# Optimization experiments

Hardware: AMD Instinct MI355X
Metric: run time of the kernel (lower is better)

The kernel has to match this reference:

```python
import jax, jax.numpy as jnp
import numpy as np

EPS_BN = 1e-5
HEADS = 4
K = 16

def _bn_eval(x, g, b, m, v):
    # eval-mode BatchNorm1d over the feature (last) axis
    return (x - m) * (g / jnp.sqrt(v + EPS_BN)) + b

def setup_inputs() -> dict:
    key = jax.random.key(0)
    ks = jax.random.split(key, 32)
    B, T, N, C = 8, 4, 2048, 11
    D = 64
    hd = D // HEADS
    s = 0.05
    rn = lambda k, shp: jax.random.normal(k, shp, jnp.float32) * s
    inp = {
        'x': jax.random.normal(ks[0], (B, T, N, C), jnp.float32),
        # PointEmbedding: Linear(11,32) + BN(32) + ReLU + Linear(32,64) + BN(64) + ReLU
        'emb_w1': rn(ks[1], (32, C)), 'emb_b1': rn(ks[2], (32,)),
        'bn1_g': jnp.ones((32,)), 'bn1_b': jnp.zeros((32,)),
        'bn1_m': rn(ks[3], (32,)), 'bn1_v': jnp.ones((32,)),
        'emb_w2': rn(ks[4], (D, 32)), 'emb_b2': rn(ks[5], (D,)),
        'bn2_g': jnp.ones((D,)), 'bn2_b': jnp.zeros((D,)),
        'bn2_m': rn(ks[6], (D,)), 'bn2_v': jnp.ones((D,)),
        # DenseGATLayer
        'gat_W': rn(ks[7], (D, D)),          # Linear(64,64,bias=False)
        'att': rn(ks[8], (HEADS, 2 * hd)),    # attention vector per head
        # TemporalCrossAttention
        'q_w': rn(ks[9], (D, D)), 'q_b': rn(ks[10], (D,)),
        'kv_w': rn(ks[11], (D, D)), 'kv_b': rn(ks[12], (D,)),
        # heads
        'lw1': rn(ks[13], (32, D)), 'lb1': rn(ks[14], (32,)),
        'lw2': rn(ks[15], (4, 32)), 'lb2': rn(ks[16], (4,)),
        'rw1': rn(ks[17], (32, D)), 'rb1': rn(ks[18], (32,)),
        'rw2': rn(ks[19], (4, 32)), 'rb2': rn(ks[20], (4,)),
    }
    return inp

def _forward(x, emb_w1, emb_b1, bn1_g, bn1_b, bn1_m, bn1_v,
             emb_w2, emb_b2, bn2_g, bn2_b, bn2_m, bn2_v,
             gat_W, att, q_w, q_b, kv_w, kv_b,
             lw1, lb1, lw2, lb2, rw1, rb1, rw2, rb2):
    B, T, N, C = x.shape
    D = gat_W.shape[0]
    hd = D // HEADS
    BT = B * T
    xf = x.reshape(BT, N, C)

    # ---- PointEmbedding (BN in eval mode) ----
    h = xf @ emb_w1.T + emb_b1
    h = jax.nn.relu(_bn_eval(h, bn1_g, bn1_b, bn1_m, bn1_v))
    h = h @ emb_w2.T + emb_b2
    h = jax.nn.relu(_bn_eval(h, bn2_g, bn2_b, bn2_m, bn2_v))  # [BT,N,D]

    # ---- DenseGATLayer ----
    pos = xf[:, :, :2]  # raw xy
    sq = jnp.sum(pos * pos, axis=-1)  # [BT,N]
    d2 = sq[:, :, None] + sq[:, None, :] - 2.0 * jnp.einsum('bnc,bmc->bnm', pos, pos)
    _, idx = jax.lax.top_k(-d2, K)  # k nearest (incl self), [BT,N,K]

    hw = (h @ gat_W.T).reshape(BT, N, HEADS, hd)  # [BT,N,H,hd]
    h_nb = jax.vmap(lambda hb, ib: hb[ib])(hw, idx)  # [BT,N,K,H,hd]

    att_self, att_nb = att[:, :hd], att[:, hd:]
    s_self = jnp.einsum('bnhd,hd->bnh', hw, att_self)       # [BT,N,H]
    s_nb = jnp.einsum('bnkhd,hd->bnkh', h_nb, att_nb)        # [BT,N,K,H]
    scores = jax.nn.leaky_relu(s_self[:, :, None, :] + s_nb, 0.2)
    alpha = jax.nn.softmax(scores, axis=2)                   # softmax over K
    out = jnp.einsum('bnkhd,bnkh->bnhd', h_nb, alpha).reshape(BT, N, D)
    h_sp = jax.nn.relu(out + h)  # [BT,N,D]

    # ---- TemporalCrossAttention ----
    ht = h_sp.reshape(B, T, N, D).transpose(0, 2, 1, 3)  # [B,N,T,D]
    Q = ht[:, :, -1, :] @ q_w.T + q_b                    # [B,N,D]
    KV = ht @ kv_w.T + kv_b                              # [B,N,T,D]
    sc = jnp.einsum('bnd,bntd->bnt', Q, KV) / jnp.sqrt(jnp.float32(D))
    w = jax.nn.softmax(sc, axis=-1)
    h_fused = jnp.einsum('bnt,bntd->bnd', w, KV)         # [B,N,D]

    # ---- heads ----
    ol = jax.nn.relu(h_fused @ lw1.T + lb1) @ lw2.T + lb2
    orr = jax.nn.relu(h_fused @ rw1.T + rb1) @ rw2.T + rb2
    lidar_mu, lidar_sigma = ol[:, :, :2], jax.nn.softplus(ol[:, :, 2:]) + 1e-6
    radar_mu, radar_sigma = orr[:, :, :2], jax.nn.softplus(orr[:, :, 2:]) + 1e-6
    return ((lidar_mu, lidar_sigma), (radar_mu, radar_sigma))

def reference(x, emb_w1, emb_b1, bn1_g, bn1_b, bn1_m, bn1_v,
              emb_w2, emb_b2, bn2_g, bn2_b, bn2_m, bn2_v,
              gat_W, att, q_w, q_b, kv_w, kv_b,
              lw1, lb1, lw2, lb2, rw1, rb1, rw2, rb2):
    return _forward(x, emb_w1, emb_b1, bn1_g, bn1_b, bn1_m, bn1_v,
                    emb_w2, emb_b2, bn2_g, bn2_b, bn2_m, bn2_v,
                    gat_W, att, q_w, q_b, kv_w, kv_b,
                    lw1, lb1, lw2, lb2, rw1, rb1, rw2, rb2)
```

## Files before the change

### kernel.cpp

```cpp
#include <hip/hip_runtime.h>
#include <math.h>

#define B_ 8
#define T_ 4
#define N_ 2048
#define C_ 11
#define D_ 64
#define H_ 4
#define HD_ 16
#define K_ 16
#define BT_ (B_*T_)

__device__ __forceinline__ float softplus_f(float x) {
    return fmaxf(x, 0.f) + log1pf(expf(-fabsf(x)));
}

__global__ __launch_bounds__(1024) void k_root(
    const float* __restrict__ x,
    const float* __restrict__ w1, const float* __restrict__ b1,
    const float* __restrict__ g1, const float* __restrict__ bb1,
    const float* __restrict__ m1, const float* __restrict__ v1,
    const float* __restrict__ w2, const float* __restrict__ b2,
    const float* __restrict__ g2, const float* __restrict__ bb2,
    const float* __restrict__ m2, const float* __restrict__ v2,
    float* __restrict__ h,
    float2* __restrict__ sp2g, int* __restrict__ sidg, int* __restrict__ fail_cnt)
{
    __shared__ unsigned long long smemU[3072];
    int t = threadIdx.x;

    if (blockIdx.x < BT_) {
        unsigned long long* kvs = smemU;
        float* lyy = (float*)(smemU + 2048);
        int bt = blockIdx.x;
        if (t == 0) fail_cnt[bt] = 0;
        const float* xb = x + (size_t)bt * N_ * C_;
        for (int m = t; m < N_; m += 1024) {
            float a = xb[m*C_], b = xb[m*C_+1];
            unsigned int bits = __float_as_uint(a);
            unsigned int u = (bits & 0x80000000u) ? ~bits : (bits | 0x80000000u);
            kvs[m] = ((unsigned long long)u << 11) | (unsigned)m;
            lyy[m] = b;
        }
        __syncthreads();
        for (int k = 2; k <= N_; k <<= 1) {
            for (int j = k >> 1; j > 0; j >>= 1) {
                int p = t;
                int i = ((p & ~(j-1)) << 1) | (p & (j-1));
                int l = i | j;
                unsigned long long a = kvs[i], b = kvs[l];
                bool asc = (i & k) == 0;
                if ((a > b) == asc) { kvs[i] = b; kvs[l] = a; }
                __syncthreads();
            }
        }
        float2* op = sp2g + (size_t)bt * N_;
        int*    oi = sidg + (size_t)bt * N_;
        for (int m = t; m < N_; m += 1024) {
            unsigned long long key = kvs[m];
            int id = (int)(key & 0x7FFull);
            unsigned int u = (unsigned int)(key >> 11);
            unsigned int bits = (u & 0x80000000u) ? (u & 0x7FFFFFFFu) : ~u;
            op[m] = make_float2(__uint_as_float(bits), lyy[id]);
            oi[m] = id;
        }
    } else {
        float* fs  = (float*)smemU;
        float* sw1 = fs;
        float* sb1 = fs + 352;
        float* sw2 = fs + 384;
        float* sb2 = fs + 2432;
        if (t < 32) {
            float s = g1[t] / sqrtf(v1[t] + 1e-5f);
            sb1[t] = (b1[t] - m1[t]) * s + bb1[t];
            for (int c = 0; c < C_; ++c) sw1[t*C_+c] = w1[t*C_+c] * s;
        } else if (t >= 64 && t < 128) {
            int j = t - 64;
            float s = g2[j] / sqrtf(v2[j] + 1e-5f);
            sb2[j] = (b2[j] - m2[j]) * s + bb2[j];
            int key = (j >> 4) & 3;
            for (int c = 0; c < 32; ++c)
                sw2[j*32 + ((((c>>2) ^ key) << 2) | (c & 3))] = w2[j*32+c] * s;
        }
        __syncthreads();

        int node = (blockIdx.x - BT_) * 256 + (t >> 2);
        int g = t & 3;
        const float* xp = x + (size_t)node * C_;
        float xin[C_];
        #pragma unroll
        for (int c = 0; c < C_; ++c) xin[c] = xp[c];

        float t1[32];
        #pragma unroll
        for (int j = 0; j < 32; ++j) {
            float a = sb1[j];
            #pragma unroll
            for (int c = 0; c < C_; ++c) a = fmaf(xin[c], sw1[j*C_+c], a);
            t1[j] = fmaxf(a, 0.f);
        }
        float4* hp4 = (float4*)(h + (size_t)node * D_ + g * 16);
        #pragma unroll
        for (int j4 = 0; j4 < 4; ++j4) {
            float o[4];
            #pragma unroll
            for (int u = 0; u < 4; ++u) {
                int j = g*16 + j4*4 + u;
                float a = sb2[j];
                #pragma unroll
                for (int c4 = 0; c4 < 8; ++c4) {
                    float4 w4 = *(const float4*)(&sw2[j*32 + ((c4 ^ g) << 2)]);
                    a = fmaf(t1[4*c4+0], w4.x, a);
                    a = fmaf(t1[4*c4+1], w4.y, a);
                    a = fmaf(t1[4*c4+2], w4.z, a);
                    a = fmaf(t1[4*c4+3], w4.w, a);
                }
                o[u] = fmaxf(a, 0.f);
            }
            hp4[j4] = make_float4(o[0], o[1], o[2], o[3]);
        }
    }
}

__global__ __launch_bounds__(256) void k_gatw_b1(
    const float* __restrict__ h, const float* __restrict__ gw,
    const float* __restrict__ att,
    float* __restrict__ hw, float* __restrict__ ssf, float* __restrict__ snbf,
    const float2* __restrict__ sp2g, const int* __restrict__ sidg,
    int* __restrict__ idx, int* __restrict__ fail_cnt, int* __restrict__ fail_lst)
{
    __shared__ float4 smemQ[1088];
    int t = threadIdx.x;

    if (blockIdx.x < BT_*N_/64) {
        float* sw   = (float*)smemQ;
        float* satA = sw + 4096;
        for (int i = t; i < D_*D_; i += 256) {
            int r = i >> 6, c = i & 63;
            sw[r*64 + ((((c>>2) ^ ((r>>4)&3)) << 2) | (c & 3))] = gw[i];
        }
        if (t < 2*H_*HD_) satA[t] = att[t];
        __syncthreads();

        int node = blockIdx.x * 64 + (t >> 2);
        int hh = t & 3;
        const float* hp = h + (size_t)node * D_;
        float hin[D_];
        #pragma unroll
        for (int j = 0; j < D_; j += 4) {
            float4 v = *(const float4*)(hp + j);
            hin[j] = v.x; hin[j+1] = v.y; hin[j+2] = v.z; hin[j+3] = v.w;
        }
        float4* wp4 = (float4*)(hw + (size_t)node * D_ + hh * HD_);
        float ss = 0.f, sn = 0.f;
        #pragma unroll
        for (int q4 = 0; q4 < 4; ++q4) {
            float o[4];
            #pragma unroll
            for (int u = 0; u < 4; ++u) {
                const int jj = q4*4 + u;
                const int j = hh*HD_ + jj;
                float a = 0.f;
                #pragma unroll
                for (int c4 = 0; c4 < D_/4; ++c4) {
                    float4 w4 = *(const float4*)(&sw[j*64 + ((c4 ^ hh) << 2)]);
                    a = fmaf(hin[4*c4+0], w4.x, a);
                    a = fmaf(hin[4*c4+1], w4.y, a);
                    a = fmaf(hin[4*c4+2], w4.z, a);
                    a = fmaf(hin[4*c4+3], w4.w, a);
                }
                o[u] = a;
                ss = fmaf(a, satA[hh*(2*HD_) + jj], ss);
                sn = fmaf(a, satA[hh*(2*HD_) + HD_ + jj], sn);
            }
            wp4[q4] = make_float4(o[0], o[1], o[2], o[3]);
        }
        ssf[(size_t)node * H_ + hh] = ss;
        snbf[(size_t)node * H_ + hh] = sn;
        return;
    }

    float2* spw = (float2*)smemQ;
    int* sidw   = (int*)((float*)smemQ + 1280);
    int* scnt   = sidw + 640;
    const int bid   = blockIdx.x - BT_*N_/64;
    const int bt    = bid >> 5;
    const int qbase = (bid & 31) << 6;
    const int base  = qbase - 288;
    const float2* pb = sp2g + (size_t)bt * N_;
    const int*    ib = sidg + (size_t)bt * N_;
    for (int L = t; L < 640; L += 256) {
        int r = base + L;
        if (r < 0 || r >= N_) { spw[L] = make_float2(1e18f, 0.f); sidw[L] = 0; }
        else { spw[L] = pb[r]; sidw[L] = ib[r]; }
    }
    if (t < 64) scnt[t] = 0;
    __syncthreads();

    const int q = t >> 2;
    const int g = t & 3;
    const int s = qbase + q;
    const int sLoc = q + 288;
    const float xs = spw[sLoc].x, ys = spw[sLoc].y;
    const float sqn = __fmaf_rn(xs, xs, __fmul_rn(ys, ys));

    float bd[K_];
    #pragma unroll
    for (int i = 0; i < K_; ++i) bd[i] = 3.402823466e38f;

    for (int i = 0; i < 8; ++i) {
        float d[16];
        #pragma unroll
        for (int j = 0; j < 16; ++j) {
            float2 p = spw[q + 32 + 64*i + 4*j + g];
            float sps = __fmaf_rn(p.x, p.x, __fmul_rn(p.y, p.y));
            float tt = __fmul_rn(xs, p.x);
            tt = __fmaf_rn(ys, p.y, tt);
            d[j] = __fmaf_rn(-2.f, tt, sps);
        }
        #pragma unroll
        for (int k = 2; k <= 16; k <<= 1) {
            #pragma unroll
            for (int jj = k >> 1; jj > 0; jj >>= 1) {
                #pragma unroll
                for (int ii = 0; ii < 16; ++ii) {
                    int ll = ii ^ jj;
                    if (ll > ii) {
                        float lo = fminf(d[ii], d[ll]);
                        float hi = fmaxf(d[ii], d[ll]);
                        if ((ii & k) == 0) { d[ii] = lo; d[ll] = hi; }
                        else               { d[ii] = hi; d[ll] = lo; }
                    }
                }
            }
        }
        #pragma unroll
        for (int ii = 0; ii < 16; ++ii) bd[ii] = fminf(bd[ii], d[15-ii]);
        #pragma unroll
        for (int jj = 8; jj > 0; jj >>= 1) {
            #pragma unroll
            for (int ii = 0; ii < 16; ++ii) {
                int ll = ii ^ jj;
                if (ll > ii) {
                    float lo = fminf(bd[ii], bd[ll]);
                    float hi = fmaxf(bd[ii], bd[ll]);
                    bd[ii] = lo; bd[ll] = hi;
                }
            }
        }
    }

    #pragma unroll
    for (int st = 1; st <= 2; st <<= 1) {
        float pr[K_];
        #pragma unroll
        for (int i = 0; i < K_; ++i) pr[i] = __shfl_xor(bd[K_-1-i], st, 64);
        #pragma unroll
        for (int i = 0; i < K_; ++i) bd[i] = fminf(bd[i], pr[i]);
        #pragma unroll
        for (int dd = 8; dd >= 1; dd >>= 1) {
            #pragma unroll
            for (int i = 0; i < K_; ++i) {
                if ((i & dd) == 0) {
                    float lo = fminf(bd[i], bd[i+dd]);
                    float hi = fmaxf(bd[i], bd[i+dd]);
                    bd[i] = lo; bd[i+dd] = hi;
                }
            }
        }
    }
    const float d15 = bd[K_-1];

    float d15s = d15 + sqn;
    float bound = d15s * 1.0001f + (sqn + 1.0f) * 1e-5f;
    bool leftOK = (s - 257 < 0);
    if (!leftOK) { float gp = xs - spw[q+31].x;  leftOK  = (gp*gp >= bound); }
    bool rightOK = (s + 256 > N_-1);
    if (!rightOK){ float gp = spw[q+544].x - xs; rightOK = (gp*gp >= bound); }
    if (!(leftOK && rightOK) && g == 0) {
        int fp = atomicAdd(&fail_cnt[bt], 1);
        fail_lst[bt*N_ + fp] = s;
    }

    int n = sidw[sLoc];
    int* op = idx + ((size_t)bt * N_ + n) * K_;
    for (int i = 0; i < 16; ++i) {
        float d[8];
        int Lb = q + 32 + 32*i + g;
        #pragma unroll
        for (int j = 0; j < 8; ++j) {
            float2 p = spw[Lb + 4*j];
            float sps = __fmaf_rn(p.x, p.x, __fmul_rn(p.y, p.y));
            float tt = __fmul_rn(xs, p.x);
            tt = __fmaf_rn(ys, p.y, tt);
            d[j] = __fmaf_rn(-2.f, tt, sps);
        }
        float dm0 = fminf(fminf(d[0],d[1]), fminf(d[2],d[3]));
        float dm1 = fminf(fminf(d[4],d[5]), fminf(d[6],d[7]));
        if (fminf(dm0, dm1) <= d15) {
            #pragma unroll
            for (int j = 0; j < 8; ++j) {
                if (d[j] <= d15) {
                    int c = atomicAdd(&scnt[q], 1);
                    if (c < K_) op[c] = sidw[Lb + 4*j];
                }
            }
        }
    }
}

__global__ __launch_bounds__(256) void k_knn_b2(const float2* __restrict__ sp2g,
    const int* __restrict__ sidg, const int* __restrict__ fail_cnt,
    const int* __restrict__ fail_lst, int* __restrict__ idx)
{
    const int bt    = blockIdx.x >> 7;
    const int chunk = blockIdx.x & 127;
    const int nf = fail_cnt[bt];
    if (chunk * 16 >= nf) return;

    __shared__ float2 sp[N_];
    __shared__ int sid[N_];
    __shared__ int scnt[16];
    const float2* pb = sp2g + (size_t)bt * N_;
    const int*    ib = sidg + (size_t)bt * N_;
    for (int m = threadIdx.x; m < N_; m += 256) { sp[m] = pb[m]; sid[m] = ib[m]; }
    if (threadIdx.x < 16) scnt[threadIdx.x] = 0;
    __syncthreads();

    const int q = threadIdx.x >> 4;
    const int g = threadIdx.x & 15;
    const bool active = (chunk*16 + q) < nf;
    const int s = active ? fail_lst[bt*N_ + chunk*16 + q] : 0;
    const float xs = sp[s].x, ys = sp[s].y;

    float bd[K_];
    #pragma unroll
    for (int i = 0; i < K_; ++i) bd[i] = 3.402823466e38f;

    for (int i = 0; i < 8; ++i) {
        float d[16];
        #pragma unroll
        for (int j = 0; j < 16; ++j) {
            float2 p = sp[256*i + 16*j + g];
            float sps = __fmaf_rn(p.x, p.x, __fmul_rn(p.y, p.y));
            float tt = __fmul_rn(xs, p.x);
            tt = __fmaf_rn(ys, p.y, tt);
            d[j] = __fmaf_rn(-2.f, tt, sps);
        }
        #pragma unroll
        for (int k = 2; k <= 16; k <<= 1) {
            #pragma unroll
            for (int jj = k >> 1; jj > 0; jj >>= 1) {
                #pragma unroll
                for (int ii = 0; ii < 16; ++ii) {
                    int ll = ii ^ jj;
                    if (ll > ii) {
                        float lo = fminf(d[ii], d[ll]);
                        float hi = fmaxf(d[ii], d[ll]);
                        if ((ii & k) == 0) { d[ii] = lo; d[ll] = hi; }
                        else               { d[ii] = hi; d[ll] = lo; }
                    }
                }
            }
        }
        #pragma unroll
        for (int ii = 0; ii < 16; ++ii) bd[ii] = fminf(bd[ii], d[15-ii]);
        #pragma unroll
        for (int jj = 8; jj > 0; jj >>= 1) {
            #pragma unroll
            for (int ii = 0; ii < 16; ++ii) {
                int ll = ii ^ jj;
                if (ll > ii) {
                    float lo = fminf(bd[ii], bd[ll]);
                    float hi = fmaxf(bd[ii], bd[ll]);
                    bd[ii] = lo; bd[ll] = hi;
                }
            }
        }
    }

    #pragma unroll
    for (int st = 1; st <= 8; st <<= 1) {
        float pr[K_];
        #pragma unroll
        for (int i = 0; i < K_; ++i) pr[i] = __shfl_xor(bd[K_-1-i], st, 64);
        #pragma unroll
        for (int i = 0; i < K_; ++i) bd[i] = fminf(bd[i], pr[i]);
        #pragma unroll
        for (int dd = 8; dd >= 1; dd >>= 1) {
            #pragma unroll
            for (int i = 0; i < K_; ++i) {
                if ((i & dd) == 0) {
                    float lo = fminf(bd[i], bd[i+dd]);
                    float hi = fmaxf(bd[i], bd[i+dd]);
                    bd[i] = lo; bd[i+dd] = hi;
                }
            }
        }
    }
    const float d15 = bd[K_-1];

    int n = sid[s];
    int* op = idx + ((size_t)bt * N_ + n) * K_;
    for (int i = 0; i < 16; ++i) {
        float d[8];
        #pragma unroll
        for (int j = 0; j < 8; ++j) {
            float2 p = sp[128*i + 16*j + g];
            float sps = __fmaf_rn(p.x, p.x, __fmul_rn(p.y, p.y));
            float tt = __fmul_rn(xs, p.x);
            tt = __fmaf_rn(ys, p.y, tt);
            d[j] = __fmaf_rn(-2.f, tt, sps);
        }
        float dm0 = fminf(fminf(d[0],d[1]), fminf(d[2],d[3]));
        float dm1 = fminf(fminf(d[4],d[5]), fminf(d[6],d[7]));
        if (active && fminf(dm0, dm1) <= d15) {
            #pragma unroll
            for (int j = 0; j < 8; ++j) {
                if (d[j] <= d15) {
                    int c = atomicAdd(&scnt[q], 1);
                    if (c < K_) op[c] = sid[128*i + 16*j + g];
                }
            }
        }
    }
}

__global__ __launch_bounds__(256, 4) void k_gat(
    const float* __restrict__ hw, const float* __restrict__ ssf,
    const float* __restrict__ snbf,
    const int* __restrict__ idx,
    float* __restrict__ h )
{
    const int t = threadIdx.x;
    const int xcd   = blockIdx.x & 7;
    const int local = blockIdx.x >> 3;
    const int btl   = local >> 5;
    const int chunk = local & 31;
    const int bt    = xcd * 4 + btl;
    const int node  = bt * N_ + chunk * 64 + (t >> 2);
    const int hh    = t & 3;

    const int* ip = idx + (size_t)node * K_;
    float ssv = ssf[(size_t)node*H_ + hh];
    const float* hwb = hw + ((size_t)bt * N_) * D_;
    const float* snb = snbf + ((size_t)bt * N_) * H_;

    int nb[K_];
    #pragma unroll
    for (int k = 0; k < K_; ++k) nb[k] = ip[k];

    float sc[K_];
    float mx = -3.402823466e38f;
    #pragma unroll
    for (int k = 0; k < K_; ++k) {
        float s = ssv + snb[(size_t)nb[k]*H_ + hh];
        s = (s >= 0.f) ? s : 0.2f * s;
        sc[k] = s;
        mx = fmaxf(mx, s);
    }
    float den = 0.f;
    #pragma unroll
    for (int k = 0; k < K_; ++k) { sc[k] = __expf(sc[k] - mx); den += sc[k]; }
    float inv = 1.f / den;

    float acc[HD_];
    #pragma unroll
    for (int i = 0; i < HD_; ++i) acc[i] = 0.f;
    #pragma unroll
    for (int k = 0; k < K_; ++k) {
        float al = sc[k] * inv;
        const float* vp = hwb + (size_t)nb[k]*D_ + hh*HD_;
        #pragma unroll
        for (int i = 0; i < HD_; i += 4) {
            float4 v = *(const float4*)(vp + i);
            acc[i]   = fmaf(v.x, al, acc[i]);
            acc[i+1] = fmaf(v.y, al, acc[i+1]);
            acc[i+2] = fmaf(v.z, al, acc[i+2]);
            acc[i+3] = fmaf(v.w, al, acc[i+3]);
        }
    }
    float4* hp4 = (float4*)(h + (size_t)node*D_ + hh*HD_);
    #pragma unroll
    for (int i4 = 0; i4 < 4; ++i4) {
        float4 old = hp4[i4];
        hp4[i4] = make_float4(fmaxf(acc[4*i4+0] + old.x, 0.f),
                              fmaxf(acc[4*i4+1] + old.y, 0.f),
                              fmaxf(acc[4*i4+2] + old.z, 0.f),
                              fmaxf(acc[4*i4+3] + old.w, 0.f));
    }
}

__global__ __launch_bounds__(256) void k_qkv(
    const float* __restrict__ hsp,
    const float* __restrict__ qw, const float* __restrict__ qb,
    const float* __restrict__ kw, const float* __restrict__ kb,
    float* __restrict__ q, float* __restrict__ kv)
{
    __shared__ float s_qw[D_*D_], s_kw[D_*D_], s_qb[D_], s_kb[D_];
    int t = threadIdx.x;
    for (int i = t; i < D_*D_; i += 256) {
        int r = i >> 6, c = i & 63;
        int p = r*64 + ((((c>>2) ^ ((r>>4)&3)) << 2) | (c & 3));
        s_qw[p] = qw[i]; s_kw[p] = kw[i];
    }
    if (t < D_) { s_qb[t] = qb[t]; s_kb[t] = kb[t]; }
    __syncthreads();

    int r = blockIdx.x * 64 + (t >> 2);
    int g = t & 3;
    const float* in; float* outp; const float* W; const float* bb;
    if (r < BT_*N_) {
        int bt = r >> 11; int n = r & (N_-1);
        int b = bt >> 2, tt = bt & 3;
        in = hsp + (size_t)r * D_;
        outp = kv + (((size_t)(b*N_ + n))*T_ + tt) * D_;
        W = s_kw; bb = s_kb;
    } else {
        int rr = r - BT_*N_;
        int b = rr >> 11, n = rr & (N_-1);
        in = hsp + ((size_t)(b*T_ + (T_-1))*N_ + n) * D_;
        outp = q + (size_t)rr * D_;
        W = s_qw; bb = s_qb;
    }
    float xin[D_];
    #pragma unroll
    for (int j = 0; j < D_; j += 4) {
        float4 v = *(const float4*)(in + j);
        xin[j] = v.x; xin[j+1] = v.y; xin[j+2] = v.z; xin[j+3] = v.w;
    }
    float4* outp4 = (float4*)(outp + g * 16);
    #pragma unroll
    for (int j4 = 0; j4 < 4; ++j4) {
        float o[4];
        #pragma unroll
        for (int u = 0; u < 4; ++u) {
            int j = g*16 + j4*4 + u;
            float a = bb[j];
            #pragma unroll
            for (int c4 = 0; c4 < D_/4; ++c4) {
                float4 w4 = *(const float4*)(&W[j*64 + ((c4 ^ g) << 2)]);
                a = fmaf(xin[4*c4+0], w4.x, a);
                a = fmaf(xin[4*c4+1], w4.y, a);
                a = fmaf(xin[4*c4+2], w4.z, a);
                a = fmaf(xin[4*c4+3], w4.w, a);
            }
            o[u] = a;
        }
        outp4[j4] = make_float4(o[0], o[1], o[2], o[3]);
    }
}

__global__ __launch_bounds__(64) void k_head(
    const float* __restrict__ q, const float* __restrict__ kv,
    const float* __restrict__ lw1, const float* __restrict__ lb1,
    const float* __restrict__ lw2, const float* __restrict__ lb2,
    const float* __restrict__ rw1, const float* __restrict__ rb1,
    const float* __restrict__ rw2, const float* __restrict__ rb2,
    float* __restrict__ out)
{
    __shared__ float sl1[32*D_], sr1[32*D_], sl2[4*32], sr2[4*32];
    __shared__ float slb1[32], srb1[32], slb2[4], srb2[4];
    int t = threadIdx.x;
    for (int i = t; i < 32*D_; i += 64) { sl1[i] = lw1[i]; sr1[i] = rw1[i]; }
    for (int i = t; i < 128; i += 64)   { sl2[i] = lw2[i]; sr2[i] = rw2[i]; }
    if (t < 32) { slb1[t] = lb1[t]; srb1[t] = rb1[t]; }
    if (t < 4)  { slb2[t] = lb2[t]; srb2[t] = rb2[t]; }
    __syncthreads();

    int rn = blockIdx.x * 64 + t;
    const float* qp = q + (size_t)rn * D_;
    const float* kp = kv + (size_t)rn * T_ * D_;

    float qv[D_];
    #pragma unroll
    for (int j = 0; j < D_; j += 4) {
        float4 v = *(const float4*)(qp + j);
        qv[j] = v.x; qv[j+1] = v.y; qv[j+2] = v.z; qv[j+3] = v.w;
    }
    float scv[T_];
    #pragma unroll
    for (int tt = 0; tt < T_; ++tt) {
        float a = 0.f;
        const float4* kr = (const float4*)(kp + tt*D_);
        #pragma unroll
        for (int c4 = 0; c4 < D_/4; ++c4) {
            float4 v = kr[c4];
            a = fmaf(qv[4*c4+0], v.x, a);
            a = fmaf(qv[4*c4+1], v.y, a);
            a = fmaf(qv[4*c4+2], v.z, a);
            a = fmaf(qv[4*c4+3], v.w, a);
        }
        scv[tt] = a * 0.125f;
    }
    float mx = fmaxf(fmaxf(scv[0], scv[1]), fmaxf(scv[2], scv[3]));
    float wsum = 0.f;
    #pragma unroll
    for (int tt = 0; tt < T_; ++tt) { scv[tt] = expf(scv[tt] - mx); wsum += scv[tt]; }
    float winv = 1.f / wsum;

    float hf[D_];
    #pragma unroll
    for (int j = 0; j < D_; ++j) hf[j] = 0.f;
    #pragma unroll
    for (int tt = 0; tt < T_; ++tt) {
        float w = scv[tt] * winv;
        const float4* kr = (const float4*)(kp + tt*D_);
        #pragma unroll
        for (int c4 = 0; c4 < D_/4; ++c4) {
            float4 v = kr[c4];
            hf[4*c4+0] = fmaf(v.x, w, hf[4*c4+0]);
            hf[4*c4+1] = fmaf(v.y, w, hf[4*c4+1]);
            hf[4*c4+2] = fmaf(v.z, w, hf[4*c4+2]);
            hf[4*c4+3] = fmaf(v.w, w, hf[4*c4+3]);
        }
    }
    float ol0 = slb2[0], ol1 = slb2[1], ol2 = slb2[2], ol3 = slb2[3];
    #pragma unroll 2
    for (int j = 0; j < 32; ++j) {
        float a = slb1[j];
        const float4* wr = (const float4*)(&sl1[j*D_]);
        #pragma unroll
        for (int c4 = 0; c4 < D_/4; ++c4) {
            float4 v = wr[c4];
            a = fmaf(hf[4*c4+0], v.x, a);
            a = fmaf(hf[4*c4+1], v.y, a);
            a = fmaf(hf[4*c4+2], v.z, a);
            a = fmaf(hf[4*c4+3], v.w, a);
        }
        a = fmaxf(a, 0.f);
        ol0 = fmaf(a, sl2[0*32+j], ol0);
        ol1 = fmaf(a, sl2[1*32+j], ol1);
        ol2 = fmaf(a, sl2[2*32+j], ol2);
        ol3 = fmaf(a, sl2[3*32+j], ol3);
    }
    float or0 = srb2[0], or1 = srb2[1], or2 = srb2[2], or3 = srb2[3];
    #pragma unroll 2
    for (int j = 0; j < 32; ++j) {
        float a = srb1[j];
        const float4* wr = (const float4*)(&sr1[j*D_]);
        #pragma unroll
        for (int c4 = 0; c4 < D_/4; ++c4) {
            float4 v = wr[c4];
            a = fmaf(hf[4*c4+0], v.x, a);
            a = fmaf(hf[4*c4+1], v.y, a);
            a = fmaf(hf[4*c4+2], v.z, a);
            a = fmaf(hf[4*c4+3], v.w, a);
        }
        a = fmaxf(a, 0.f);
        or0 = fmaf(a, sr2[0*32+j], or0);
        or1 = fmaf(a, sr2[1*32+j], or1);
        or2 = fmaf(a, sr2[2*32+j], or2);
        or3 = fmaf(a, sr2[3*32+j], or3);
    }
    const int NB = B_ * N_;
    out[0*2*NB + rn*2 + 0] = ol0;
    out[0*2*NB + rn*2 + 1] = ol1;
    out[1*2*NB + rn*2 + 0] = softplus_f(ol2) + 1e-6f;
    out[1*2*NB + rn*2 + 1] = softplus_f(ol3) + 1e-6f;
    out[2*2*NB + rn*2 + 0] = or0;
    out[2*2*NB + rn*2 + 1] = or1;
    out[3*2*NB + rn*2 + 0] = softplus_f(or2) + 1e-6f;
    out[3*2*NB + rn*2 + 1] = softplus_f(or3) + 1e-6f;
}

extern "C" void kernel_launch(void* const* d_in, const int* in_sizes, int n_in,
                              void* d_out, int out_size, void* d_ws, size_t ws_size,
                              hipStream_t stream)
{
    const float* x   = (const float*)d_in[0];
    const float* ew1 = (const float*)d_in[1];
    const float* eb1 = (const float*)d_in[2];
    const float* g1  = (const float*)d_in[3];
    const float* bb1 = (const float*)d_in[4];
    const float* m1  = (const float*)d_in[5];
    const float* v1  = (const float*)d_in[6];
    const float* ew2 = (const float*)d_in[7];
    const float* eb2 = (const float*)d_in[8];
    const float* g2  = (const float*)d_in[9];
    const float* bb2 = (const float*)d_in[10];
    const float* m2  = (const float*)d_in[11];
    const float* v2  = (const float*)d_in[12];
    const float* gw  = (const float*)d_in[13];
    const float* att = (const float*)d_in[14];
    const float* qw  = (const float*)d_in[15];
    const float* qb  = (const float*)d_in[16];
    const float* kw  = (const float*)d_in[17];
    const float* kb  = (const float*)d_in[18];
    const float* lw1 = (const float*)d_in[19];
    const float* lb1 = (const float*)d_in[20];
    const float* lw2 = (const float*)d_in[21];
    const float* lb2 = (const float*)d_in[22];
    const float* rw1 = (const float*)d_in[23];
    const float* rb1 = (const float*)d_in[24];
    const float* rw2 = (const float*)d_in[25];
    const float* rb2 = (const float*)d_in[26];
    float* out = (float*)d_out;

    const size_t NTOT = (size_t)BT_*N_;
    float* h    = (float*)d_ws;
    float* hw   = h   + NTOT*D_;
    float* kvb  = hw  + NTOT*D_;
    float* ssf  = kvb + NTOT*D_;
    float* snbf = ssf + NTOT*H_;
    int*   idx  = (int*)(snbf + NTOT*H_);
    float* q    = (float*)(idx + NTOT*K_);
    float2* sp2g = (float2*)(q + (size_t)B_*N_*D_);
    int*   sidg = (int*)((float*)sp2g + 2*NTOT);
    int*   fail_cnt = sidg + NTOT;
    int*   fail_lst = fail_cnt + 32;

    k_root<<<BT_ + BT_*N_/256, 1024, 0, stream>>>(x, ew1, eb1, g1, bb1, m1, v1,
                                                  ew2, eb2, g2, bb2, m2, v2,
                                                  h, sp2g, sidg, fail_cnt);
    k_gatw_b1<<<BT_*N_/64 + BT_*(N_/64), 256, 0, stream>>>(
        h, gw, att, hw, ssf, snbf, sp2g, sidg, idx, fail_cnt, fail_lst);
    k_knn_b2<<<BT_*128, 256, 0, stream>>>(sp2g, sidg, fail_cnt, fail_lst, idx);
    k_gat<<<(BT_*N_*H_)/256, 256, 0, stream>>>(hw, ssf, snbf, idx, h);
    k_qkv<<<(BT_*N_ + B_*N_)/64, 256, 0, stream>>>(h, qw, qb, kw, kb, q, kvb);
    k_head<<<(B_*N_)/64, 64, 0, stream>>>(q, kvb, lw1, lb1, lw2, lb2,
                                          rw1, rb1, rw2, rb2, out);
}
```

Baseline: 210.6 us.

## Prune kNN candidate blocks using early threshold and nearest-first block order

The kNN distance scan now visits candidate blocks starting from the centre and moving outward. After two blocks it merges the partial top-K across the four lanes of a query to get a K-th-distance threshold. Later blocks are sorted and merged only if some lane in the wavefront has a distance below that threshold, so bitonic sorts on blocks that cannot contribute are skipped. In exchange it adds an extra cross-lane merge and a wavefront vote, and the benefit depends on how spatially sorted the points are.

```diff
diff --git a/kernel.cpp b/kernel.cpp
--- a/kernel.cpp
+++ b/kernel.cpp
@@ -208,7 +208,10 @@
     #pragma unroll
     for (int i = 0; i < K_; ++i) bd[i] = 3.402823466e38f;
 
-    for (int i = 0; i < 8; ++i) {
+    float thr = 3.402823466e38f;
+    for (int io = 0; io < 8; ++io) {
+        const int i = (io < 2) ? (4 - io)
+                    : ((io & 1) ? (3 - (io >> 1)) : (4 + (io >> 1)));
         float d[16];
         #pragma unroll
         for (int j = 0; j < 16; ++j) {
@@ -218,35 +221,71 @@
             tt = __fmaf_rn(ys, p.y, tt);
             d[j] = __fmaf_rn(-2.f, tt, sps);
         }
-        #pragma unroll
-        for (int k = 2; k <= 16; k <<= 1) {
-            #pragma unroll
-            for (int jj = k >> 1; jj > 0; jj >>= 1) {
+        bool doSort = true;
+        if (io >= 2) {
+            float bmn = fminf(
+                fminf(fminf(fminf(d[0],d[1]),fminf(d[2],d[3])),
+                      fminf(fminf(d[4],d[5]),fminf(d[6],d[7]))),
+                fminf(fminf(fminf(d[8],d[9]),fminf(d[10],d[11])),
+                      fminf(fminf(d[12],d[13]),fminf(d[14],d[15]))));
+            doSort = !__all(bmn >= thr);
+        }
+        if (doSort) {
+            #pragma unroll
+            for (int k = 2; k <= 16; k <<= 1) {
+                #pragma unroll
+                for (int jj = k >> 1; jj > 0; jj >>= 1) {
+                    #pragma unroll
+                    for (int ii = 0; ii < 16; ++ii) {
+                        int ll = ii ^ jj;
+                        if (ll > ii) {
+                            float lo = fminf(d[ii], d[ll]);
+                            float hi = fmaxf(d[ii], d[ll]);
+                            if ((ii & k) == 0) { d[ii] = lo; d[ll] = hi; }
+                            else               { d[ii] = hi; d[ll] = lo; }
+                        }
+                    }
+                }
+            }
+            #pragma unroll
+            for (int ii = 0; ii < 16; ++ii) bd[ii] = fminf(bd[ii], d[15-ii]);
+            #pragma unroll
+            for (int jj = 8; jj > 0; jj >>= 1) {
                 #pragma unroll
                 for (int ii = 0; ii < 16; ++ii) {
                     int ll = ii ^ jj;
                     if (ll > ii) {
-                        float lo = fminf(d[ii], d[ll]);
-                        float hi = fmaxf(d[ii], d[ll]);
-                        if ((ii & k) == 0) { d[ii] = lo; d[ll] = hi; }
-                        else               { d[ii] = hi; d[ll] = lo; }
+                        float lo = fminf(bd[ii], bd[ll]);
+                        float hi = fmaxf(bd[ii], bd[ll]);
+                        bd[ii] = lo; bd[ll] = hi;
                     }
                 }
             }
         }
-        #pragma unroll
-        for (int ii = 0; ii < 16; ++ii) bd[ii] = fminf(bd[ii], d[15-ii]);
-        #pragma unroll
-        for (int jj = 8; jj > 0; jj >>= 1) {
-            #pragma unroll
-            for (int ii = 0; ii < 16; ++ii) {
-                int ll = ii ^ jj;
-                if (ll > ii) {
-                    float lo = fminf(bd[ii], bd[ll]);
-                    float hi = fmaxf(bd[ii], bd[ll]);
-                    bd[ii] = lo; bd[ll] = hi;
-                }
-            }
+        if (io == 1) {
+            float tm[K_];
+            #pragma unroll
+            for (int ii = 0; ii < K_; ++ii) tm[ii] = bd[ii];
+            #pragma unroll
+            for (int st = 1; st <= 2; st <<= 1) {
+                float pr[K_];
+                #pragma unroll
+                for (int ii = 0; ii < K_; ++ii) pr[ii] = __shfl_xor(tm[K_-1-ii], st, 64);
+                #pragma unroll
+                for (int ii = 0; ii < K_; ++ii) tm[ii] = fminf(tm[ii], pr[ii]);
+                #pragma unroll
+                for (int dd = 8; dd >= 1; dd >>= 1) {
+                    #pragma unroll
+                    for (int ii = 0; ii < K_; ++ii) {
+                        if ((ii & dd) == 0) {
+                            float lo = fminf(tm[ii], tm[ii+dd]);
+                            float hi = fmaxf(tm[ii], tm[ii+dd]);
+                            tm[ii] = lo; tm[ii+dd] = hi;
+                        }
+                    }
+                }
+            }
+            thr = tm[K_-1];
         }
     }
 
```

Result: no change. 214.4 us (+1.8%).
